# Kernel tuning notes

Hardware: AMD Instinct MI355X
Metric: run time of the kernel (lower is better)

The kernel has to match this reference:

```python
import jax, jax.numpy as jnp
import numpy as np

B, G, K, A = 2, 50000, 32, 64  # batch, grid points, neighbors, ao_vals


def setup_inputs() -> dict:
    key = jax.random.key(0)
    k1, k2, k3, k4 = jax.random.split(key, 4)
    out = jax.random.normal(k1, (B, G, A), dtype=jnp.float32)
    # neighbor indices in [0, G]; index G points at the zero padding row
    coords_neighbors_idx = jax.random.randint(k2, (G, K), 0, G + 1, dtype=jnp.int32)
    scale = 1.0 / np.sqrt(A)
    W2 = jax.random.normal(k3, (A, A), dtype=jnp.float32) * scale
    b2 = jnp.zeros((A,), dtype=jnp.float32)
    W3 = jax.random.normal(k4, (A, A), dtype=jnp.float32) * scale
    b3 = jnp.zeros((A,), dtype=jnp.float32)
    return {"out": out, "coords_neighbors_idx": coords_neighbors_idx,
            "W2": W2, "b2": b2, "W3": W3, "b3": b3}


def reference(out, coords_neighbors_idx, W2, b2, W3, b3):
    n_batch, n_grid, n_ao = out.shape
    # pad grid axis with a zero row so index n_grid gathers zeros
    pad = jnp.concatenate([out, jnp.zeros((n_batch, 1, n_ao), out.dtype)], axis=1)
    # gather neighbors: [B, G, K, A], then sum-aggregate over neighbors
    messages = jnp.take(pad, coords_neighbors_idx, axis=1).sum(axis=2)  # [B, G, A]
    messages = messages @ W2 + b2  # dense_2 (activation=None)
    y = out + messages             # residual
    y = y @ W3 + b3                # dense_3 (activation=None)
    return y
```

## Files before the change

### kernel.cpp

```cpp
#include <hip/hip_runtime.h>
#include <hip/hip_fp16.h>


constexpr int A  = 64;
constexpr int K  = 32;
constexpr int GPB = 32;
constexpr int XS = 136;

typedef _Float16 f16x8 __attribute__((ext_vector_type(8)));
typedef float    f32x4 __attribute__((ext_vector_type(4)));

__global__ void wprep_kernel(const float* __restrict__ W2, const float* __restrict__ b2,
                             const float* __restrict__ W3, const float* __restrict__ b3,
                             __half* __restrict__ WTg, float* __restrict__ bb) {
  const int e = blockIdx.x * 256 + threadIdx.x;
  const int n = e >> 6, k = e & 63;
  float acc = 0.f;
#pragma unroll
  for (int q = 0; q < A; ++q) acc = fmaf(W2[k * A + q], W3[q * A + n], acc);
  WTg[n * 128 + k]     = __float2half(acc);
  WTg[n * 128 + A + k] = __float2half(W3[k * A + n]);
  if (blockIdx.x == 0 && threadIdx.x < A) {
    const int t = threadIdx.x;
    float b = b3[t];
#pragma unroll
    for (int q = 0; q < A; ++q) b = fmaf(b2[q], W3[q * A + t], b);
    bb[t] = b;
  }
}

__global__ void pack_kernel(const float2* __restrict__ out2,
                            __half2* __restrict__ packed, const int G) {
  const int d = blockIdx.x * 256 + threadIdx.x;
  const int total = (G + 1) * 64;
  if (d >= total) return;
  const int g = d >> 6, c = d & 63;
  float2 v = make_float2(0.f, 0.f);
  if (g < G) {
    const int b = c >> 5;
    v = out2[(size_t)b * (G * 32) + (size_t)g * 32 + (c & 31)];
  }
  packed[d] = __floats2half2_rn(v.x, v.y);
}

__global__ __launch_bounds__(256, 4) void fused_kernel(
    const __half2* __restrict__ packed, const int* __restrict__ nbr,
    const __half* __restrict__ WTg, const float* __restrict__ bb,
    float* __restrict__ y, const int G) {
  __shared__ __half X[64 * XS];
  __shared__ __half WT[64 * XS];

  const int tid = threadIdx.x;

  {
    const unsigned int* src = (const unsigned int*)WTg;
    unsigned int* dst = (unsigned int*)WT;
#pragma unroll
    for (int s = 0; s < 16; ++s) {
      const int d = s * 256 + tid;
      const int n = d >> 6, c = d & 63;
      dst[n * (XS / 2) + c] = src[d];
    }
  }

  const int lane = tid & 63;
  const int w = __builtin_amdgcn_readfirstlane(tid >> 6);
  const int gbase = blockIdx.x * GPB;
  const int gcount = min(GPB, G - gbase);
  const int e = lane & 31;
  const int rb = (lane >> 5) * 32;

  const __half2 z = __floats2half2_rn(0.f, 0.f);

#pragma unroll
  for (int gg = 0; gg < 8; ++gg) {
    const int gl = w * 8 + gg;
    if (gl < gcount) {
      const int g = gbase + gl;
      const int* np = nbr + g * K;
      __half2 m0 = z, m1 = z, m2 = z, m3 = z;
#pragma unroll
      for (int k = 0; k < K; k += 4) {
        const __half2 u0 = packed[(size_t)np[k]     * 64 + lane];
        const __half2 u1 = packed[(size_t)np[k + 1] * 64 + lane];
        const __half2 u2 = packed[(size_t)np[k + 2] * 64 + lane];
        const __half2 u3 = packed[(size_t)np[k + 3] * 64 + lane];
        m0 = __hadd2(m0, u0);
        m1 = __hadd2(m1, u1);
        m2 = __hadd2(m2, u2);
        m3 = __hadd2(m3, u3);
      }
      const __half2 m = __hadd2(__hadd2(m0, m1), __hadd2(m2, m3));
      const __half2 o = packed[(size_t)g * 64 + lane];
      const int r = rb + gl;
      *(__half2*)&X[r * XS + 2 * e]     = m;
      *(__half2*)&X[r * XS + A + 2 * e] = o;
    }
  }
  __syncthreads();

  const int quad = lane >> 4;
  const int mn = lane & 15;
  f32x4 acc0 = {0.f, 0.f, 0.f, 0.f};
  f32x4 acc1 = {0.f, 0.f, 0.f, 0.f};
  f32x4 acc2 = {0.f, 0.f, 0.f, 0.f};
  f32x4 acc3 = {0.f, 0.f, 0.f, 0.f};
#pragma unroll
  for (int kt = 0; kt < 4; ++kt) {
    const int ko = kt * 32 + quad * 8;
    const f16x8 a = *(const f16x8*)&X[(w * 16 + mn) * XS + ko];
    const f16x8 b0 = *(const f16x8*)&WT[(0 * 16 + mn) * XS + ko];
    acc0 = __builtin_amdgcn_mfma_f32_16x16x32_f16(a, b0, acc0, 0, 0, 0);
    const f16x8 b1 = *(const f16x8*)&WT[(1 * 16 + mn) * XS + ko];
    acc1 = __builtin_amdgcn_mfma_f32_16x16x32_f16(a, b1, acc1, 0, 0, 0);
    const f16x8 b2 = *(const f16x8*)&WT[(2 * 16 + mn) * XS + ko];
    acc2 = __builtin_amdgcn_mfma_f32_16x16x32_f16(a, b2, acc2, 0, 0, 0);
    const f16x8 b3 = *(const f16x8*)&WT[(3 * 16 + mn) * XS + ko];
    acc3 = __builtin_amdgcn_mfma_f32_16x16x32_f16(a, b3, acc3, 0, 0, 0);
  }

  f32x4 accs[4] = {acc0, acc1, acc2, acc3};
#pragma unroll
  for (int nt = 0; nt < 4; ++nt) {
    const int col = nt * 16 + mn;
    const float bv = bb[col];
#pragma unroll
    for (int rg = 0; rg < 4; ++rg) {
      const int row = w * 16 + quad * 4 + rg;
      const int b = row >> 5, gl = row & 31;
      if (gl < gcount)
        y[((size_t)b * G + (gbase + gl)) * 64 + col] = accs[nt][rg] + bv;
    }
  }
}

extern "C" void kernel_launch(void* const* d_in, const int* in_sizes, int n_in,
                              void* d_out, int out_size, void* d_ws, size_t ws_size,
                              hipStream_t stream) {
  const float* out = (const float*)d_in[0];
  const int*   nbr = (const int*)d_in[1];
  const float* W2  = (const float*)d_in[2];
  const float* b2  = (const float*)d_in[3];
  const float* W3  = (const float*)d_in[4];
  const float* b3  = (const float*)d_in[5];
  float* y = (float*)d_out;
  const int G = in_sizes[1] / K;

  __half2* packed = (__half2*)d_ws;
  const size_t packedBytes = (size_t)(G + 1) * 64 * sizeof(__half2);
  __half* WTg = (__half*)((char*)d_ws + packedBytes);
  float* bb = (float*)((char*)d_ws + packedBytes + 8192 * sizeof(__half));

  wprep_kernel<<<16, 256, 0, stream>>>(W2, b2, W3, b3, WTg, bb);

  const int packTotal = (G + 1) * 64;
  pack_kernel<<<(packTotal + 255) / 256, 256, 0, stream>>>(
      (const float2*)out, packed, G);

  const int blocks = (G + GPB - 1) / GPB;
  fused_kernel<<<blocks, 256, 0, stream>>>(packed, nbr, WTg, bb, y, G);
}
```

Baseline: 144.4 us.

## Bucket neighbor indices by slice and process slices in lockstep for L2 locality

Adds a sort kernel that groups each grid point's neighbor indices into 13 slices of 4096 rows, padding each slice to an even count. The fused kernel now runs a fixed 1024 persistent blocks, each handling about 49 grid points. All waves sweep the slices together, so the random gathers from the packed table stay within a smaller working set that fits in cache. It also removes the shared-memory staging of the weights and reads B fragments straight from global memory. The cost is an extra sort pass over the neighbor array, per-point variable-length inner loops built on readlane, and a hardcoded slice count that assumes G is at most about 53K.

New measurement: 227.6 us. +57.6%, slower.

```diff
diff --git a/kernel.cpp b/kernel.cpp
--- a/kernel.cpp
+++ b/kernel.cpp
@@ -4,8 +4,12 @@
 
 constexpr int A  = 64;
 constexpr int K  = 32;
-constexpr int GPB = 32;
+constexpr int NB = 1024;
+constexpr int NSLICE = 13;
+constexpr int SLOTS  = 48;
 constexpr int XS = 136;
+constexpr int XROWS = 112;
+constexpr int MAXGW = 13;
 
 typedef _Float16 f16x8 __attribute__((ext_vector_type(8)));
 typedef float    f32x4 __attribute__((ext_vector_type(4)));
@@ -32,104 +36,143 @@
 __global__ void pack_kernel(const float2* __restrict__ out2,
                             __half2* __restrict__ packed, const int G) {
   const int d = blockIdx.x * 256 + threadIdx.x;
-  const int total = (G + 1) * 64;
-  if (d >= total) return;
+  if (d >= (G + 1) * 64) return;
   const int g = d >> 6, c = d & 63;
   float2 v = make_float2(0.f, 0.f);
-  if (g < G) {
-    const int b = c >> 5;
-    v = out2[(size_t)b * (G * 32) + (size_t)g * 32 + (c & 31)];
-  }
+  if (g < G) v = out2[(size_t)(c >> 5) * (G * 32) + (size_t)g * 32 + (c & 31)];
   packed[d] = __floats2half2_rn(v.x, v.y);
 }
 
+__global__ void sort_kernel(const int* __restrict__ nbr, int* __restrict__ sorted,
+                            int4* __restrict__ offs, const int G) {
+  const int g = blockIdx.x * 256 + threadIdx.x;
+  if (g >= G) return;
+  int v[K];
+#pragma unroll
+  for (int k = 0; k < K; ++k) v[k] = nbr[g * K + k];
+  int* dst = sorted + (size_t)g * SLOTS;
+  unsigned b[NSLICE + 1];
+  b[0] = 0;
+  int pos = 0;
+#pragma unroll
+  for (int s = 0; s < NSLICE; ++s) {
+    const int start = pos;
+#pragma unroll
+    for (int k = 0; k < K; ++k)
+      if ((v[k] >> 12) == s) dst[pos++] = v[k];
+    if ((pos - start) & 1) dst[pos++] = G;
+    b[s + 1] = (unsigned)(pos >> 1);
+  }
+  int4 o;
+  o.x = (int)(b[0]  | (b[1]  << 8) | (b[2]  << 16) | (b[3]  << 24));
+  o.y = (int)(b[4]  | (b[5]  << 8) | (b[6]  << 16) | (b[7]  << 24));
+  o.z = (int)(b[8]  | (b[9]  << 8) | (b[10] << 16) | (b[11] << 24));
+  o.w = (int)(b[12] | (b[13] << 8));
+  offs[g] = o;
+}
+
+__device__ __forceinline__ int rl(int v, int l) {
+  return __builtin_amdgcn_readlane(v, l);
+}
+
 __global__ __launch_bounds__(256, 4) void fused_kernel(
-    const __half2* __restrict__ packed, const int* __restrict__ nbr,
-    const __half* __restrict__ WTg, const float* __restrict__ bb,
-    float* __restrict__ y, const int G) {
-  __shared__ __half X[64 * XS];
-  __shared__ __half WT[64 * XS];
+    const __half2* __restrict__ packed, const int* __restrict__ sorted,
+    const int4* __restrict__ offs, const __half* __restrict__ WTg,
+    const float* __restrict__ bb, float* __restrict__ y, const int G) {
+  __shared__ __half X[XROWS * XS];
 
   const int tid = threadIdx.x;
-
-  {
-    const unsigned int* src = (const unsigned int*)WTg;
-    unsigned int* dst = (unsigned int*)WT;
-#pragma unroll
-    for (int s = 0; s < 16; ++s) {
-      const int d = s * 256 + tid;
-      const int n = d >> 6, c = d & 63;
-      dst[n * (XS / 2) + c] = src[d];
-    }
-  }
-
   const int lane = tid & 63;
-  const int w = __builtin_amdgcn_readfirstlane(tid >> 6);
-  const int gbase = blockIdx.x * GPB;
-  const int gcount = min(GPB, G - gbase);
-  const int e = lane & 31;
-  const int rb = (lane >> 5) * 32;
-
+  const int w = tid >> 6;
+  const int bid = blockIdx.x;
+  const int g0 = (int)(((long long)bid * G) / NB);
+  const int g1 = (int)(((long long)(bid + 1) * G) / NB);
+  const int NR = g1 - g0;
+  const int w0 = g0 + (NR * w) / 4;
+  const int w1 = g0 + (NR * (w + 1)) / 4;
+  const int ng = w1 - w0;
+
+  int idxv[MAXGW];
+  int4 po4[MAXGW];
+  __half2 acc[MAXGW];
   const __half2 z = __floats2half2_rn(0.f, 0.f);
-
-#pragma unroll
-  for (int gg = 0; gg < 8; ++gg) {
-    const int gl = w * 8 + gg;
-    if (gl < gcount) {
-      const int g = gbase + gl;
-      const int* np = nbr + g * K;
-      __half2 m0 = z, m1 = z, m2 = z, m3 = z;
-#pragma unroll
-      for (int k = 0; k < K; k += 4) {
-        const __half2 u0 = packed[(size_t)np[k]     * 64 + lane];
-        const __half2 u1 = packed[(size_t)np[k + 1] * 64 + lane];
-        const __half2 u2 = packed[(size_t)np[k + 2] * 64 + lane];
-        const __half2 u3 = packed[(size_t)np[k + 3] * 64 + lane];
-        m0 = __hadd2(m0, u0);
-        m1 = __hadd2(m1, u1);
-        m2 = __hadd2(m2, u2);
-        m3 = __hadd2(m3, u3);
+  const int lslot = lane < SLOTS ? lane : SLOTS - 1;
+#pragma unroll
+  for (int gi = 0; gi < MAXGW; ++gi) {
+    acc[gi] = z;
+    if (gi < ng) {
+      idxv[gi] = sorted[(size_t)(w0 + gi) * SLOTS + lslot];
+      po4[gi] = offs[w0 + gi];
+    } else {
+      idxv[gi] = G;
+      po4[gi] = make_int4(0, 0, 0, 0);
+    }
+  }
+
+#pragma unroll
+  for (int s = 0; s < NSLICE; ++s) {
+#pragma unroll
+    for (int gi = 0; gi < MAXGW; ++gi) {
+      if (gi < ng) {
+        const unsigned pb[4] = {(unsigned)po4[gi].x, (unsigned)po4[gi].y,
+                                (unsigned)po4[gi].z, (unsigned)po4[gi].w};
+        const int p0 = (int)((pb[s >> 2] >> ((s & 3) * 8)) & 255u);
+        const int p1 = (int)((pb[(s + 1) >> 2] >> (((s + 1) & 3) * 8)) & 255u);
+        for (int p = p0; p < p1; ++p) {
+          const int i0 = rl(idxv[gi], 2 * p);
+          const int i1 = rl(idxv[gi], 2 * p + 1);
+          const __half2 u0 = packed[(size_t)i0 * 64 + lane];
+          const __half2 u1 = packed[(size_t)i1 * 64 + lane];
+          acc[gi] = __hadd2(acc[gi], u0);
+          acc[gi] = __hadd2(acc[gi], u1);
+        }
       }
-      const __half2 m = __hadd2(__hadd2(m0, m1), __hadd2(m2, m3));
-      const __half2 o = packed[(size_t)g * 64 + lane];
-      const int r = rb + gl;
-      *(__half2*)&X[r * XS + 2 * e]     = m;
-      *(__half2*)&X[r * XS + A + 2 * e] = o;
+    }
+  }
+
+  const int e2 = 2 * (lane & 31);
+  const int rb = (lane >> 5) * 56;
+#pragma unroll
+  for (int gi = 0; gi < MAXGW; ++gi) {
+    if (gi < ng) {
+      const int gl = (w0 - g0) + gi;
+      const int row = rb + gl;
+      *(__half2*)&X[row * XS + e2] = acc[gi];
+      *(__half2*)&X[row * XS + A + e2] = packed[(size_t)(w0 + gi) * 64 + lane];
     }
   }
   __syncthreads();
 
-  const int quad = lane >> 4;
-  const int mn = lane & 15;
-  f32x4 acc0 = {0.f, 0.f, 0.f, 0.f};
-  f32x4 acc1 = {0.f, 0.f, 0.f, 0.f};
-  f32x4 acc2 = {0.f, 0.f, 0.f, 0.f};
-  f32x4 acc3 = {0.f, 0.f, 0.f, 0.f};
-#pragma unroll
-  for (int kt = 0; kt < 4; ++kt) {
-    const int ko = kt * 32 + quad * 8;
-    const f16x8 a = *(const f16x8*)&X[(w * 16 + mn) * XS + ko];
-    const f16x8 b0 = *(const f16x8*)&WT[(0 * 16 + mn) * XS + ko];
-    acc0 = __builtin_amdgcn_mfma_f32_16x16x32_f16(a, b0, acc0, 0, 0, 0);
-    const f16x8 b1 = *(const f16x8*)&WT[(1 * 16 + mn) * XS + ko];
-    acc1 = __builtin_amdgcn_mfma_f32_16x16x32_f16(a, b1, acc1, 0, 0, 0);
-    const f16x8 b2 = *(const f16x8*)&WT[(2 * 16 + mn) * XS + ko];
-    acc2 = __builtin_amdgcn_mfma_f32_16x16x32_f16(a, b2, acc2, 0, 0, 0);
-    const f16x8 b3 = *(const f16x8*)&WT[(3 * 16 + mn) * XS + ko];
-    acc3 = __builtin_amdgcn_mfma_f32_16x16x32_f16(a, b3, acc3, 0, 0, 0);
-  }
-
-  f32x4 accs[4] = {acc0, acc1, acc2, acc3};
-#pragma unroll
-  for (int nt = 0; nt < 4; ++nt) {
-    const int col = nt * 16 + mn;
-    const float bv = bb[col];
-#pragma unroll
-    for (int rg = 0; rg < 4; ++rg) {
-      const int row = w * 16 + quad * 4 + rg;
-      const int b = row >> 5, gl = row & 31;
-      if (gl < gcount)
-        y[((size_t)b * G + (gbase + gl)) * 64 + col] = accs[nt][rg] + bv;
+  const int quad = lane >> 4, mn = lane & 15;
+#pragma unroll
+  for (int j = 0; j < 2; ++j) {
+    const int t = w + 4 * j;
+    if (t < 7) {
+      f32x4 ac[4] = {{0.f, 0.f, 0.f, 0.f}, {0.f, 0.f, 0.f, 0.f},
+                     {0.f, 0.f, 0.f, 0.f}, {0.f, 0.f, 0.f, 0.f}};
+#pragma unroll
+      for (int kt = 0; kt < 4; ++kt) {
+        const int ko = kt * 32 + quad * 8;
+        const f16x8 a = *(const f16x8*)&X[(t * 16 + mn) * XS + ko];
+#pragma unroll
+        for (int nt = 0; nt < 4; ++nt) {
+          const f16x8 bfr = *(const f16x8*)&WTg[(nt * 16 + mn) * 128 + ko];
+          ac[nt] = __builtin_amdgcn_mfma_f32_16x16x32_f16(a, bfr, ac[nt], 0, 0, 0);
+        }
+      }
+#pragma unroll
+      for (int nt = 0; nt < 4; ++nt) {
+        const int col = nt * 16 + mn;
+        const float bv = bb[col];
+#pragma unroll
+        for (int rg = 0; rg < 4; ++rg) {
+          const int row = t * 16 + quad * 4 + rg;
+          const int bt = row >= 56 ? 1 : 0;
+          const int gl = row - 56 * bt;
+          if (gl < NR)
+            y[((size_t)bt * G + (g0 + gl)) * 64 + col] = ac[nt][rg] + bv;
+        }
+      }
     }
   }
 }
@@ -147,16 +190,20 @@
   const int G = in_sizes[1] / K;
 
   __half2* packed = (__half2*)d_ws;
-  const size_t packedBytes = (size_t)(G + 1) * 64 * sizeof(__half2);
-  __half* WTg = (__half*)((char*)d_ws + packedBytes);
-  float* bb = (float*)((char*)d_ws + packedBytes + 8192 * sizeof(__half));
-
-  wprep_kernel<<<16, 256, 0, stream>>>(W2, b2, W3, b3, WTg, bb);
+  const size_t pbytes = (size_t)(G + 1) * 64 * sizeof(__half2);
+  int4* offs = (int4*)((char*)d_ws + pbytes);
+  int* sorted = (int*)((char*)d_ws + pbytes + (size_t)G * sizeof(int4));
+  __half* WTg = (__half*)((char*)d_ws + pbytes + (size_t)G * sizeof(int4) +
+                          (size_t)G * SLOTS * sizeof(int));
+  float* bbp = (float*)(WTg + 128 * 64);
+
+  wprep_kernel<<<16, 256, 0, stream>>>(W2, b2, W3, b3, WTg, bbp);
 
   const int packTotal = (G + 1) * 64;
   pack_kernel<<<(packTotal + 255) / 256, 256, 0, stream>>>(
       (const float2*)out, packed, G);
 
-  const int blocks = (G + GPB - 1) / GPB;
-  fused_kernel<<<blocks, 256, 0, stream>>>(packed, nbr, WTg, bb, y, G);
-}
+  sort_kernel<<<(G + 255) / 256, 256, 0, stream>>>(nbr, sorted, offs, G);
+
+  fused_kernel<<<NB, 256, 0, stream>>>(packed, sorted, offs, WTg, bbp, y, G);
+}
```
